# Optimization experiments

Measured on AMD Instinct MI355X. Metric: run time of the kernel, lower is better.

Reference implementation:

```python
import jax, jax.numpy as jnp
import numpy as np

L, C, S = 4096, 128, 64
SAMPLE_RATE = 4096.0  # Hz; dt offset is 1/sample_rate as in the flax module


def setup_inputs() -> dict:
    key = jax.random.key(0)
    ks = jax.random.split(key, 4)
    x = jax.random.normal(ks[0], (L, C), dtype=jnp.float32)
    # S4D-real init: A = -arange(1, S+1), param stores log(-A) broadcast to (C, S)
    A_log = jnp.broadcast_to(
        jnp.log(jnp.arange(1, S + 1, dtype=jnp.float32)), (C, S)
    )
    sc = 1.0 / np.sqrt(C)  # lecun_normal-like scale for Dense kernels
    B_kernel = (jax.random.normal(ks[1], (C, S)) * sc).astype(jnp.float32)
    B_bias = jnp.zeros((S,), jnp.float32)
    C_kernel = (jax.random.normal(ks[2], (C, S)) * sc).astype(jnp.float32)
    C_bias = jnp.zeros((S,), jnp.float32)
    dt_kernel = (jax.random.normal(ks[3], (C, C)) * sc).astype(jnp.float32)
    dt_bias = jnp.zeros((C,), jnp.float32)
    return {
        "x": x,
        "A_log": A_log,
        "B_kernel": B_kernel,
        "B_bias": B_bias,
        "C_kernel": C_kernel,
        "C_bias": C_bias,
        "dt_kernel": dt_kernel,
        "dt_bias": dt_bias,
    }


def reference(x, A_log, B_kernel, B_bias, C_kernel, C_bias, dt_kernel, dt_bias):
    # ssm params
    A = -jnp.exp(A_log)                                   # (C, S), negative real
    B = 1.0 + x @ B_kernel + B_bias                       # (L, S)
    Cm = x @ C_kernel + C_bias                            # (L, S)
    dt = jax.nn.softplus(1.0 / SAMPLE_RATE + x @ dt_kernel + dt_bias)  # (L, C)
    # discretization (ZOH for diagonal real A)
    At = jnp.exp(A[None, :, :] * dt[:, :, None])          # (L, C, S)
    ut = (At - 1.0) * (B[:, None, :] / A[None, :, :]) * x[:, :, None]  # (L, C, S)

    # parallel linear-recurrence scan: h_t = At_t * h_{t-1} + ut_t, h0 = 0
    def comb(e1, e2):
        a1, u1 = e1
        a2, u2 = e2
        return (a2 * a1, a2 * u1 + u2)

    _, ht = jax.lax.associative_scan(comb, (At, ut))      # scans over axis 0 (L)
    y = jnp.einsum("ls,lcs->lc", Cm, ht)                  # (L, C)
    return y
```

## Files before the change

kernel.cpp:

```cpp
#include <hip/hip_runtime.h>
#include <math.h>

#define LL 4096
#define CC 128
#define SS 64
#define NCH 128
#define CLEN 32
#define CS 8192
#define GW 8
#define NG 16

__global__ __launch_bounds__(256) void k_proj(
    const float* __restrict__ x,
    const float* __restrict__ Bk, const float* __restrict__ Bb,
    const float* __restrict__ Ck, const float* __restrict__ Cb,
    const float* __restrict__ Dk, const float* __restrict__ Db,
    float* __restrict__ Bmat, float* __restrict__ Cmat,
    float* __restrict__ DTmT, float* __restrict__ xT)
{
    __shared__ float xs[CC][20];
    const int r0 = blockIdx.x * 16;
    const int t = threadIdx.x;
    {
        const int r = t >> 4, k8 = (t & 15) * 8;
        const float4 v0 = *(const float4*)&x[(r0 + r) * CC + k8];
        const float4 v1 = *(const float4*)&x[(r0 + r) * CC + k8 + 4];
        xs[k8+0][r] = v0.x; xs[k8+1][r] = v0.y; xs[k8+2][r] = v0.z; xs[k8+3][r] = v0.w;
        xs[k8+4][r] = v1.x; xs[k8+5][r] = v1.y; xs[k8+6][r] = v1.z; xs[k8+7][r] = v1.w;
    }
    __syncthreads();
    {
        const int k = t >> 1, half = (t & 1) * 8;
        const float4 a = *(const float4*)&xs[k][half];
        const float4 b = *(const float4*)&xs[k][half + 4];
        *(float4*)&xT[k * LL + r0 + half]     = a;
        *(float4*)&xT[k * LL + r0 + half + 4] = b;
    }
    const int tc = t & 63, tr = t >> 6;
    const float* Wb; int wstride, wo;
    if (tc < 16)      { Wb = Bk; wstride = SS; wo = 4 * tc; }
    else if (tc < 32) { Wb = Ck; wstride = SS; wo = 4 * tc - 64; }
    else              { Wb = Dk; wstride = CC; wo = 4 * tc - 128; }
    float acc[4][4];
#pragma unroll
    for (int r = 0; r < 4; ++r)
#pragma unroll
        for (int j = 0; j < 4; ++j) acc[r][j] = 0.0f;
    for (int k = 0; k < CC; ++k) {
        const float4 wq = *(const float4*)(Wb + k * wstride + wo);
        const float4 xq = *(const float4*)&xs[k][4 * tr];
        const float wv[4] = {wq.x, wq.y, wq.z, wq.w};
        const float xv[4] = {xq.x, xq.y, xq.z, xq.w};
#pragma unroll
        for (int r = 0; r < 4; ++r)
#pragma unroll
            for (int j = 0; j < 4; ++j) acc[r][j] = fmaf(xv[r], wv[j], acc[r][j]);
    }
    const int rb = r0 + 4 * tr;
    if (tc < 32) {
        const float* bb = (tc < 16) ? Bb : Cb;
        const float add = (tc < 16) ? 1.0f : 0.0f;
        float bias[4];
#pragma unroll
        for (int j = 0; j < 4; ++j) bias[j] = add + bb[wo + j];
        float* dst = (tc < 16) ? Bmat : Cmat;
#pragma unroll
        for (int r = 0; r < 4; ++r) {
            const float4 o = make_float4(acc[r][0] + bias[0], acc[r][1] + bias[1],
                                         acc[r][2] + bias[2], acc[r][3] + bias[3]);
            *(float4*)&dst[(rb + r) * SS + wo] = o;
        }
    } else {
#pragma unroll
        for (int j = 0; j < 4; ++j) {
            const float bj = Db[wo + j] + 0.000244140625f;
            float sp[4];
#pragma unroll
            for (int r = 0; r < 4; ++r) {
                const float z = acc[r][j] + bj;
                sp[r] = fmaxf(z, 0.0f) + log1pf(__expf(-fabsf(z)));
            }
            *(float4*)&DTmT[(wo + j) * LL + rb] = make_float4(sp[0], sp[1], sp[2], sp[3]);
        }
    }
}

__global__ __launch_bounds__(512) void k_chunk(
    const float* __restrict__ xT, const float* __restrict__ A_log,
    const float* __restrict__ Bmat, const float* __restrict__ DTmT,
    float* __restrict__ Ea, float* __restrict__ Eu,
    float* __restrict__ Ga, float* __restrict__ Gu)
{
    __shared__ float2 agg[GW][SS];
    const int lane = threadIdx.x & 63;
    const int w = threadIdx.x >> 6;
    const int c = blockIdx.x >> 4;
    const int g = blockIdx.x & (NG - 1);
    const int ch = __builtin_amdgcn_readfirstlane(g * GW + w);
    const float A = -__expf(A_log[c * SS + lane]);
    const float invA = 1.0f / A;
    const int l0 = ch * CLEN;
    const float* dtp = DTmT + c * LL + l0;
    const float* xp  = xT   + c * LL + l0;
    const float* Bp  = Bmat + l0 * SS + lane;
    float ap = 1.0f, uc = 0.0f;
#pragma unroll
    for (int i = 0; i < CLEN; ++i) {
        const float dtl = dtp[i];
        const float xl  = xp[i];
        const float Bl  = Bp[i * SS];
        const float At  = __expf(A * dtl);
        const float u   = (At - 1.0f) * invA * (Bl * xl);
        ap *= At;
        uc = fmaf(At, uc, u);
    }
    agg[w][lane] = make_float2(ap, uc);
    __syncthreads();
    float ea = 1.0f, eu = 0.0f;
    for (int k = 0; k < w; ++k) {
        const float2 tt = agg[k][lane];
        eu = fmaf(tt.x, eu, tt.y);
        ea *= tt.x;
    }
    const int j = c * SS + lane;
    Ea[ch * CS + j] = ea;
    Eu[ch * CS + j] = eu;
    if (w == GW - 1) {
        const float2 tt = agg[GW - 1][lane];
        Gu[g * CS + j] = fmaf(tt.x, eu, tt.y);
        Ga[g * CS + j] = ea * tt.x;
    }
}

__global__ __launch_bounds__(256) void k_mid(
    const float* __restrict__ Ga, const float* __restrict__ Gu,
    float* __restrict__ hG)
{
    const int j = blockIdx.x * 256 + threadIdx.x;
    float h = 0.0f;
#pragma unroll
    for (int g = 0; g < NG; ++g) {
        hG[g * CS + j] = h;
        h = fmaf(Ga[g * CS + j], h, Gu[g * CS + j]);
    }
}

__global__ __launch_bounds__(256) void k_emit(
    const float* __restrict__ xT, const float* __restrict__ A_log,
    const float* __restrict__ Bmat, const float* __restrict__ Cmat,
    const float* __restrict__ DTmT,
    const float* __restrict__ Ea, const float* __restrict__ Eu,
    const float* __restrict__ hG,
    float* __restrict__ y)
{
    const int lane = threadIdx.x & 63;
    const int gw = blockIdx.x * 4 + (threadIdx.x >> 6);
    const int c  = __builtin_amdgcn_readfirstlane(gw & (CC - 1));
    const int ch = __builtin_amdgcn_readfirstlane(gw >> 7);
    const int g  = ch >> 3;
    const float A = -__expf(A_log[c * SS + lane]);
    const float invA = 1.0f / A;
    const int l0 = ch * CLEN;
    const int j = c * SS + lane;
    const float* dtp = DTmT + c * LL + l0;
    const float* xp  = xT   + c * LL + l0;
    const float* Bp  = Bmat + l0 * SS + lane;
    const float* Cp  = Cmat + l0 * SS + lane;
    float h = fmaf(Ea[ch * CS + j], hG[g * CS + j], Eu[ch * CS + j]);
    float p[CLEN];
#pragma unroll
    for (int i = 0; i < CLEN; ++i) {
        const float dtl = dtp[i];
        const float xl  = xp[i];
        const float Bl  = Bp[i * SS];
        const float Cl  = Cp[i * SS];
        const float At  = __expf(A * dtl);
        const float u   = (At - 1.0f) * invA * (Bl * xl);
        h = fmaf(At, h, u);
        p[i] = Cl * h;
    }
#pragma unroll
    for (int k = 0; k < 5; ++k) {
        const int d = 1 << k;
        const bool hi = (lane & d) != 0;
#pragma unroll
        for (int i = 0; i < (CLEN >> (k + 1)); ++i) {
            const float a = p[2 * i], b = p[2 * i + 1];
            const float send = hi ? a : b;
            const float t = __shfl_xor(send, d, 64);
            p[i] = (hi ? b : a) + t;
        }
    }
    const float t = __shfl_xor(p[0], 32, 64);
    const float yv = p[0] + t;
    if (lane < 32) y[(l0 + lane) * CC + c] = yv;
}

extern "C" void kernel_launch(void* const* d_in, const int* in_sizes, int n_in,
                              void* d_out, int out_size, void* d_ws, size_t ws_size,
                              hipStream_t stream)
{
    const float* x  = (const float*)d_in[0];
    const float* Al = (const float*)d_in[1];
    const float* Bk = (const float*)d_in[2];
    const float* Bb = (const float*)d_in[3];
    const float* Ck = (const float*)d_in[4];
    const float* Cb = (const float*)d_in[5];
    const float* Dk = (const float*)d_in[6];
    const float* Db = (const float*)d_in[7];
    float* y  = (float*)d_out;
    float* ws = (float*)d_ws;

    float* Bmat = ws;
    float* Cmat = Bmat + LL * SS;
    float* DTmT = Cmat + LL * SS;
    float* xT   = DTmT + CC * LL;
    float* Ea   = xT   + CC * LL;
    float* Eu   = Ea   + NCH * CS;
    float* Ga   = Eu   + NCH * CS;
    float* Gu   = Ga   + NG * CS;
    float* hG   = Gu   + NG * CS;

    k_proj <<<LL / 16,           256, 0, stream>>>(x, Bk, Bb, Ck, Cb, Dk, Db, Bmat, Cmat, DTmT, xT);
    k_chunk<<<CC * NG,           512, 0, stream>>>(xT, Al, Bmat, DTmT, Ea, Eu, Ga, Gu);
    k_mid  <<<CS / 256,          256, 0, stream>>>(Ga, Gu, hG);
    k_emit <<<(NCH * CS) / 256,  256, 0, stream>>>(xT, Al, Bmat, Cmat, DTmT, Ea, Eu, hG, y);
}
```

Before: 58.30 us.

## Fuse group-prefix scan into emit, drop per-chunk carries, shrink projection tiles

Removes the k_mid kernel and the Ea/Eu per-chunk buffers. k_agg now writes only group aggregates. k_emit recomputes each chunk's aggregate in shared memory, rebuilds the intra-group prefix, and serially folds the preceding group aggregates to get its starting state. This saves one launch and the global round trips of per-chunk carries, at the cost of recomputing the chunk exponentials in emit. The projection kernel now computes 4 rows per block with a 1x4 register tile instead of 16 rows with 4x4, giving more blocks but less weight reuse per load.

```diff
diff --git a/kernel.cpp b/kernel.cpp
--- a/kernel.cpp
+++ b/kernel.cpp
@@ -18,177 +18,152 @@
     float* __restrict__ Bmat, float* __restrict__ Cmat,
     float* __restrict__ DTmT, float* __restrict__ xT)
 {
-    __shared__ float xs[CC][20];
-    const int r0 = blockIdx.x * 16;
+    __shared__ float xs[CC][4];
+    const int r0 = blockIdx.x * 4;
     const int t = threadIdx.x;
     {
-        const int r = t >> 4, k8 = (t & 15) * 8;
-        const float4 v0 = *(const float4*)&x[(r0 + r) * CC + k8];
-        const float4 v1 = *(const float4*)&x[(r0 + r) * CC + k8 + 4];
-        xs[k8+0][r] = v0.x; xs[k8+1][r] = v0.y; xs[k8+2][r] = v0.z; xs[k8+3][r] = v0.w;
-        xs[k8+4][r] = v1.x; xs[k8+5][r] = v1.y; xs[k8+6][r] = v1.z; xs[k8+7][r] = v1.w;
+        const int r = t >> 6, k2 = (t & 63) * 2;
+        const float2 v = *(const float2*)&x[(r0 + r) * CC + k2];
+        xs[k2][r] = v.x; xs[k2 + 1][r] = v.y;
     }
     __syncthreads();
-    {
-        const int k = t >> 1, half = (t & 1) * 8;
-        const float4 a = *(const float4*)&xs[k][half];
-        const float4 b = *(const float4*)&xs[k][half + 4];
-        *(float4*)&xT[k * LL + r0 + half]     = a;
-        *(float4*)&xT[k * LL + r0 + half + 4] = b;
+    if (t < CC) {
+        *(float4*)&xT[t * LL + r0] = *(const float4*)&xs[t][0];
     }
     const int tc = t & 63, tr = t >> 6;
     const float* Wb; int wstride, wo;
     if (tc < 16)      { Wb = Bk; wstride = SS; wo = 4 * tc; }
     else if (tc < 32) { Wb = Ck; wstride = SS; wo = 4 * tc - 64; }
     else              { Wb = Dk; wstride = CC; wo = 4 * tc - 128; }
-    float acc[4][4];
-#pragma unroll
-    for (int r = 0; r < 4; ++r)
-#pragma unroll
-        for (int j = 0; j < 4; ++j) acc[r][j] = 0.0f;
+    float acc[4] = {0.f, 0.f, 0.f, 0.f};
+#pragma unroll 8
     for (int k = 0; k < CC; ++k) {
         const float4 wq = *(const float4*)(Wb + k * wstride + wo);
-        const float4 xq = *(const float4*)&xs[k][4 * tr];
-        const float wv[4] = {wq.x, wq.y, wq.z, wq.w};
-        const float xv[4] = {xq.x, xq.y, xq.z, xq.w};
-#pragma unroll
-        for (int r = 0; r < 4; ++r)
-#pragma unroll
-            for (int j = 0; j < 4; ++j) acc[r][j] = fmaf(xv[r], wv[j], acc[r][j]);
+        const float xv = xs[k][tr];
+        acc[0] = fmaf(xv, wq.x, acc[0]);
+        acc[1] = fmaf(xv, wq.y, acc[1]);
+        acc[2] = fmaf(xv, wq.z, acc[2]);
+        acc[3] = fmaf(xv, wq.w, acc[3]);
     }
-    const int rb = r0 + 4 * tr;
-    if (tc < 32) {
-        const float* bb = (tc < 16) ? Bb : Cb;
-        const float add = (tc < 16) ? 1.0f : 0.0f;
-        float bias[4];
-#pragma unroll
-        for (int j = 0; j < 4; ++j) bias[j] = add + bb[wo + j];
-        float* dst = (tc < 16) ? Bmat : Cmat;
-#pragma unroll
-        for (int r = 0; r < 4; ++r) {
-            const float4 o = make_float4(acc[r][0] + bias[0], acc[r][1] + bias[1],
-                                         acc[r][2] + bias[2], acc[r][3] + bias[3]);
-            *(float4*)&dst[(rb + r) * SS + wo] = o;
-        }
+    const int row = r0 + tr;
+    if (tc < 16) {
+        const float4 o = make_float4(acc[0] + 1.0f + Bb[wo], acc[1] + 1.0f + Bb[wo+1],
+                                     acc[2] + 1.0f + Bb[wo+2], acc[3] + 1.0f + Bb[wo+3]);
+        *(float4*)&Bmat[row * SS + wo] = o;
+    } else if (tc < 32) {
+        const float4 o = make_float4(acc[0] + Cb[wo], acc[1] + Cb[wo+1],
+                                     acc[2] + Cb[wo+2], acc[3] + Cb[wo+3]);
+        *(float4*)&Cmat[row * SS + wo] = o;
     } else {
 #pragma unroll
         for (int j = 0; j < 4; ++j) {
-            const float bj = Db[wo + j] + 0.000244140625f;
-            float sp[4];
-#pragma unroll
-            for (int r = 0; r < 4; ++r) {
-                const float z = acc[r][j] + bj;
-                sp[r] = fmaxf(z, 0.0f) + log1pf(__expf(-fabsf(z)));
-            }
-            *(float4*)&DTmT[(wo + j) * LL + rb] = make_float4(sp[0], sp[1], sp[2], sp[3]);
+            const float z = acc[j] + Db[wo + j] + 0.000244140625f;
+            const float sp = fmaxf(z, 0.0f) + log1pf(__expf(-fabsf(z)));
+            DTmT[(wo + j) * LL + row] = sp;
         }
     }
 }
 
-__global__ __launch_bounds__(512) void k_chunk(
+__global__ __launch_bounds__(512, 4) void k_agg(
     const float* __restrict__ xT, const float* __restrict__ A_log,
     const float* __restrict__ Bmat, const float* __restrict__ DTmT,
-    float* __restrict__ Ea, float* __restrict__ Eu,
     float* __restrict__ Ga, float* __restrict__ Gu)
 {
-    __shared__ float2 agg[GW][SS];
+    __shared__ float2 sagg[GW][SS];
     const int lane = threadIdx.x & 63;
-    const int w = threadIdx.x >> 6;
+    const int w = __builtin_amdgcn_readfirstlane(threadIdx.x >> 6);
     const int c = blockIdx.x >> 4;
     const int g = blockIdx.x & (NG - 1);
-    const int ch = __builtin_amdgcn_readfirstlane(g * GW + w);
-    const float A = -__expf(A_log[c * SS + lane]);
+    const int j = c * SS + lane;
+    const float A = -__expf(A_log[j]);
     const float invA = 1.0f / A;
-    const int l0 = ch * CLEN;
+    const int l0 = (g * GW + w) * CLEN;
     const float* dtp = DTmT + c * LL + l0;
     const float* xp  = xT   + c * LL + l0;
     const float* Bp  = Bmat + l0 * SS + lane;
     float ap = 1.0f, uc = 0.0f;
 #pragma unroll
     for (int i = 0; i < CLEN; ++i) {
-        const float dtl = dtp[i];
-        const float xl  = xp[i];
-        const float Bl  = Bp[i * SS];
-        const float At  = __expf(A * dtl);
-        const float u   = (At - 1.0f) * invA * (Bl * xl);
+        const float At = __expf(A * dtp[i]);
+        const float u  = (At - 1.0f) * invA * (Bp[i * SS] * xp[i]);
         ap *= At;
         uc = fmaf(At, uc, u);
     }
-    agg[w][lane] = make_float2(ap, uc);
+    sagg[w][lane] = make_float2(ap, uc);
     __syncthreads();
-    float ea = 1.0f, eu = 0.0f;
-    for (int k = 0; k < w; ++k) {
-        const float2 tt = agg[k][lane];
-        eu = fmaf(tt.x, eu, tt.y);
-        ea *= tt.x;
-    }
-    const int j = c * SS + lane;
-    Ea[ch * CS + j] = ea;
-    Eu[ch * CS + j] = eu;
-    if (w == GW - 1) {
-        const float2 tt = agg[GW - 1][lane];
-        Gu[g * CS + j] = fmaf(tt.x, eu, tt.y);
-        Ga[g * CS + j] = ea * tt.x;
+    if (w == 0) {
+        float ga = 1.0f, gu = 0.0f;
+#pragma unroll
+        for (int k = 0; k < GW; ++k) {
+            const float2 t = sagg[k][lane];
+            gu = fmaf(t.x, gu, t.y);
+            ga *= t.x;
+        }
+        Ga[g * CS + j] = ga;
+        Gu[g * CS + j] = gu;
     }
 }
 
-__global__ __launch_bounds__(256) void k_mid(
-    const float* __restrict__ Ga, const float* __restrict__ Gu,
-    float* __restrict__ hG)
-{
-    const int j = blockIdx.x * 256 + threadIdx.x;
-    float h = 0.0f;
-#pragma unroll
-    for (int g = 0; g < NG; ++g) {
-        hG[g * CS + j] = h;
-        h = fmaf(Ga[g * CS + j], h, Gu[g * CS + j]);
-    }
-}
-
-__global__ __launch_bounds__(256) void k_emit(
+__global__ __launch_bounds__(512, 4) void k_emit(
     const float* __restrict__ xT, const float* __restrict__ A_log,
     const float* __restrict__ Bmat, const float* __restrict__ Cmat,
     const float* __restrict__ DTmT,
-    const float* __restrict__ Ea, const float* __restrict__ Eu,
-    const float* __restrict__ hG,
+    const float* __restrict__ Ga, const float* __restrict__ Gu,
     float* __restrict__ y)
 {
+    __shared__ float2 sagg[GW][SS];
     const int lane = threadIdx.x & 63;
-    const int gw = blockIdx.x * 4 + (threadIdx.x >> 6);
-    const int c  = __builtin_amdgcn_readfirstlane(gw & (CC - 1));
-    const int ch = __builtin_amdgcn_readfirstlane(gw >> 7);
-    const int g  = ch >> 3;
-    const float A = -__expf(A_log[c * SS + lane]);
+    const int w = __builtin_amdgcn_readfirstlane(threadIdx.x >> 6);
+    const int c = blockIdx.x >> 4;
+    const int g = blockIdx.x & (NG - 1);
+    const int j = c * SS + lane;
+    const float A = -__expf(A_log[j]);
     const float invA = 1.0f / A;
-    const int l0 = ch * CLEN;
-    const int j = c * SS + lane;
+    float hg = 0.0f;
+    for (int gg = 0; gg < g; ++gg)
+        hg = fmaf(Ga[gg * CS + j], hg, Gu[gg * CS + j]);
+    const int l0 = (g * GW + w) * CLEN;
     const float* dtp = DTmT + c * LL + l0;
     const float* xp  = xT   + c * LL + l0;
     const float* Bp  = Bmat + l0 * SS + lane;
     const float* Cp  = Cmat + l0 * SS + lane;
-    float h = fmaf(Ea[ch * CS + j], hG[g * CS + j], Eu[ch * CS + j]);
+    {
+        float ap = 1.0f, uc = 0.0f;
+#pragma unroll
+        for (int i = 0; i < CLEN; ++i) {
+            const float At = __expf(A * dtp[i]);
+            const float u  = (At - 1.0f) * invA * (Bp[i * SS] * xp[i]);
+            ap *= At;
+            uc = fmaf(At, uc, u);
+        }
+        sagg[w][lane] = make_float2(ap, uc);
+    }
+    __syncthreads();
+    float ea = 1.0f, eu = 0.0f;
+    for (int k = 0; k < w; ++k) {
+        const float2 t = sagg[k][lane];
+        eu = fmaf(t.x, eu, t.y);
+        ea *= t.x;
+    }
+    float h = fmaf(ea, hg, eu);
     float p[CLEN];
 #pragma unroll
     for (int i = 0; i < CLEN; ++i) {
-        const float dtl = dtp[i];
-        const float xl  = xp[i];
-        const float Bl  = Bp[i * SS];
-        const float Cl  = Cp[i * SS];
-        const float At  = __expf(A * dtl);
-        const float u   = (At - 1.0f) * invA * (Bl * xl);
+        const float At = __expf(A * dtp[i]);
+        const float u  = (At - 1.0f) * invA * (Bp[i * SS] * xp[i]);
         h = fmaf(At, h, u);
-        p[i] = Cl * h;
+        p[i] = Cp[i * SS] * h;
     }
 #pragma unroll
     for (int k = 0; k < 5; ++k) {
         const int d = 1 << k;
         const bool hi = (lane & d) != 0;
 #pragma unroll
-        for (int i = 0; i < (CLEN >> (k + 1)); ++i) {
-            const float a = p[2 * i], b = p[2 * i + 1];
+        for (int i2 = 0; i2 < (CLEN >> (k + 1)); ++i2) {
+            const float a = p[2 * i2], b = p[2 * i2 + 1];
             const float send = hi ? a : b;
             const float t = __shfl_xor(send, d, 64);
-            p[i] = (hi ? b : a) + t;
+            p[i2] = (hi ? b : a) + t;
         }
     }
     const float t = __shfl_xor(p[0], 32, 64);
@@ -215,14 +190,10 @@
     float* Cmat = Bmat + LL * SS;
     float* DTmT = Cmat + LL * SS;
     float* xT   = DTmT + CC * LL;
-    float* Ea   = xT   + CC * LL;
-    float* Eu   = Ea   + NCH * CS;
-    float* Ga   = Eu   + NCH * CS;
+    float* Ga   = xT   + CC * LL;
     float* Gu   = Ga   + NG * CS;
-    float* hG   = Gu   + NG * CS;
 
-    k_proj <<<LL / 16,           256, 0, stream>>>(x, Bk, Bb, Ck, Cb, Dk, Db, Bmat, Cmat, DTmT, xT);
-    k_chunk<<<CC * NG,           512, 0, stream>>>(xT, Al, Bmat, DTmT, Ea, Eu, Ga, Gu);
-    k_mid  <<<CS / 256,          256, 0, stream>>>(Ga, Gu, hG);
-    k_emit <<<(NCH * CS) / 256,  256, 0, stream>>>(xT, Al, Bmat, Cmat, DTmT, Ea, Eu, hG, y);
+    k_proj<<<LL / 4,  256, 0, stream>>>(x, Bk, Bb, Ck, Cb, Dk, Db, Bmat, Cmat, DTmT, xT);
+    k_agg <<<CC * NG, 512, 0, stream>>>(xT, Al, Bmat, DTmT, Ga, Gu);
+    k_emit<<<CC * NG, 512, 0, stream>>>(xT, Al, Bmat, Cmat, DTmT, Ga, Gu, y);
 }
```

After: 65.23 us. +11.9%, slower.

## Merge mid-scan into emit kernel and drop per-chunk carry buffers

Applied to the files above, without the earlier changes.

Removes the separate group-carry kernel and the per-chunk Ea/Eu workspace arrays. The first sweep now writes only per-group aggregates. The emit kernel redoes the intra-group chunk aggregation in shared memory and serially combines up to 15 group aggregates per thread to get its starting state. This saves one launch and the global traffic for chunk carries, at the cost of recomputing chunk aggregates and extra register pressure from holding the at/uu arrays.

```diff
diff --git a/kernel.cpp b/kernel.cpp
--- a/kernel.cpp
+++ b/kernel.cpp
@@ -4,11 +4,10 @@
 #define LL 4096
 #define CC 128
 #define SS 64
-#define NCH 128
 #define CLEN 32
-#define CS 8192
 #define GW 8
 #define NG 16
+#define CS 8192
 
 __global__ __launch_bounds__(256) void k_proj(
     const float* __restrict__ x,
@@ -85,114 +84,117 @@
     }
 }
 
-__global__ __launch_bounds__(512) void k_chunk(
+__global__ __launch_bounds__(512, 4) void k_sweep1(
     const float* __restrict__ xT, const float* __restrict__ A_log,
     const float* __restrict__ Bmat, const float* __restrict__ DTmT,
-    float* __restrict__ Ea, float* __restrict__ Eu,
     float* __restrict__ Ga, float* __restrict__ Gu)
 {
     __shared__ float2 agg[GW][SS];
     const int lane = threadIdx.x & 63;
-    const int w = threadIdx.x >> 6;
+    const int w = __builtin_amdgcn_readfirstlane(threadIdx.x >> 6);
     const int c = blockIdx.x >> 4;
     const int g = blockIdx.x & (NG - 1);
-    const int ch = __builtin_amdgcn_readfirstlane(g * GW + w);
-    const float A = -__expf(A_log[c * SS + lane]);
+    const int j = c * SS + lane;
+    const float A = -__expf(A_log[j]);
     const float invA = 1.0f / A;
-    const int l0 = ch * CLEN;
+    const int l0 = (g * GW + w) * CLEN;
     const float* dtp = DTmT + c * LL + l0;
     const float* xp  = xT   + c * LL + l0;
     const float* Bp  = Bmat + l0 * SS + lane;
     float ap = 1.0f, uc = 0.0f;
 #pragma unroll
     for (int i = 0; i < CLEN; ++i) {
-        const float dtl = dtp[i];
-        const float xl  = xp[i];
-        const float Bl  = Bp[i * SS];
-        const float At  = __expf(A * dtl);
-        const float u   = (At - 1.0f) * invA * (Bl * xl);
+        const float At = __expf(A * dtp[i]);
+        const float u  = (At - 1.0f) * invA * (Bp[i * SS] * xp[i]);
         ap *= At;
         uc = fmaf(At, uc, u);
     }
     agg[w][lane] = make_float2(ap, uc);
     __syncthreads();
-    float ea = 1.0f, eu = 0.0f;
-    for (int k = 0; k < w; ++k) {
-        const float2 tt = agg[k][lane];
-        eu = fmaf(tt.x, eu, tt.y);
-        ea *= tt.x;
-    }
-    const int j = c * SS + lane;
-    Ea[ch * CS + j] = ea;
-    Eu[ch * CS + j] = eu;
-    if (w == GW - 1) {
-        const float2 tt = agg[GW - 1][lane];
-        Gu[g * CS + j] = fmaf(tt.x, eu, tt.y);
-        Ga[g * CS + j] = ea * tt.x;
-    }
-}
-
-__global__ __launch_bounds__(256) void k_mid(
-    const float* __restrict__ Ga, const float* __restrict__ Gu,
-    float* __restrict__ hG)
-{
-    const int j = blockIdx.x * 256 + threadIdx.x;
-    float h = 0.0f;
-#pragma unroll
-    for (int g = 0; g < NG; ++g) {
-        hG[g * CS + j] = h;
-        h = fmaf(Ga[g * CS + j], h, Gu[g * CS + j]);
-    }
-}
-
-__global__ __launch_bounds__(256) void k_emit(
+    if (w == 0) {
+        float ga = 1.0f, gu = 0.0f;
+#pragma unroll
+        for (int k = 0; k < GW; ++k) {
+            const float2 t = agg[k][lane];
+            gu = fmaf(t.x, gu, t.y);
+            ga *= t.x;
+        }
+        Ga[g * CS + j] = ga;
+        Gu[g * CS + j] = gu;
+    }
+}
+
+__global__ __launch_bounds__(512, 4) void k_emit(
     const float* __restrict__ xT, const float* __restrict__ A_log,
     const float* __restrict__ Bmat, const float* __restrict__ Cmat,
     const float* __restrict__ DTmT,
-    const float* __restrict__ Ea, const float* __restrict__ Eu,
-    const float* __restrict__ hG,
+    const float* __restrict__ Ga, const float* __restrict__ Gu,
     float* __restrict__ y)
 {
+    __shared__ float2 agg[GW][SS];
     const int lane = threadIdx.x & 63;
-    const int gw = blockIdx.x * 4 + (threadIdx.x >> 6);
-    const int c  = __builtin_amdgcn_readfirstlane(gw & (CC - 1));
-    const int ch = __builtin_amdgcn_readfirstlane(gw >> 7);
-    const int g  = ch >> 3;
-    const float A = -__expf(A_log[c * SS + lane]);
+    const int w = __builtin_amdgcn_readfirstlane(threadIdx.x >> 6);
+    const int c = blockIdx.x >> 4;
+    const int g = blockIdx.x & (NG - 1);
+    const int j = c * SS + lane;
+    const float A = -__expf(A_log[j]);
     const float invA = 1.0f / A;
-    const int l0 = ch * CLEN;
-    const int j = c * SS + lane;
+    float hg = 0.0f;
+    {
+        float gar[NG - 1], gur[NG - 1];
+#pragma unroll
+        for (int gg = 0; gg < NG - 1; ++gg) {
+            gar[gg] = Ga[gg * CS + j];
+            gur[gg] = Gu[gg * CS + j];
+        }
+#pragma unroll
+        for (int gg = 0; gg < NG - 1; ++gg)
+            hg = (gg < g) ? fmaf(gar[gg], hg, gur[gg]) : hg;
+    }
+    const int l0 = (g * GW + w) * CLEN;
     const float* dtp = DTmT + c * LL + l0;
     const float* xp  = xT   + c * LL + l0;
     const float* Bp  = Bmat + l0 * SS + lane;
     const float* Cp  = Cmat + l0 * SS + lane;
-    float h = fmaf(Ea[ch * CS + j], hG[g * CS + j], Eu[ch * CS + j]);
-    float p[CLEN];
+    float at[CLEN], uu[CLEN];
+    {
+        float ap = 1.0f, uc = 0.0f;
+#pragma unroll
+        for (int i = 0; i < CLEN; ++i) {
+            at[i] = __expf(A * dtp[i]);
+            uu[i] = (at[i] - 1.0f) * invA * (Bp[i * SS] * xp[i]);
+            ap *= at[i];
+            uc = fmaf(at[i], uc, uu[i]);
+        }
+        agg[w][lane] = make_float2(ap, uc);
+    }
+    __syncthreads();
+    float ea = 1.0f, eu = 0.0f;
+    for (int k = 0; k < w; ++k) {
+        const float2 t = agg[k][lane];
+        eu = fmaf(t.x, eu, t.y);
+        ea *= t.x;
+    }
+    float h = fmaf(ea, hg, eu);
 #pragma unroll
     for (int i = 0; i < CLEN; ++i) {
-        const float dtl = dtp[i];
-        const float xl  = xp[i];
-        const float Bl  = Bp[i * SS];
-        const float Cl  = Cp[i * SS];
-        const float At  = __expf(A * dtl);
-        const float u   = (At - 1.0f) * invA * (Bl * xl);
-        h = fmaf(At, h, u);
-        p[i] = Cl * h;
+        h = fmaf(at[i], h, uu[i]);
+        uu[i] = Cp[i * SS] * h;
     }
 #pragma unroll
     for (int k = 0; k < 5; ++k) {
         const int d = 1 << k;
         const bool hi = (lane & d) != 0;
 #pragma unroll
-        for (int i = 0; i < (CLEN >> (k + 1)); ++i) {
-            const float a = p[2 * i], b = p[2 * i + 1];
+        for (int i2 = 0; i2 < (CLEN >> (k + 1)); ++i2) {
+            const float a = uu[2 * i2], b = uu[2 * i2 + 1];
             const float send = hi ? a : b;
             const float t = __shfl_xor(send, d, 64);
-            p[i] = (hi ? b : a) + t;
-        }
-    }
-    const float t = __shfl_xor(p[0], 32, 64);
-    const float yv = p[0] + t;
+            uu[i2] = (hi ? b : a) + t;
+        }
+    }
+    const float t = __shfl_xor(uu[0], 32, 64);
+    const float yv = uu[0] + t;
     if (lane < 32) y[(l0 + lane) * CC + c] = yv;
 }
 
@@ -215,14 +217,10 @@
     float* Cmat = Bmat + LL * SS;
     float* DTmT = Cmat + LL * SS;
     float* xT   = DTmT + CC * LL;
-    float* Ea   = xT   + CC * LL;
-    float* Eu   = Ea   + NCH * CS;
-    float* Ga   = Eu   + NCH * CS;
+    float* Ga   = xT   + CC * LL;
     float* Gu   = Ga   + NG * CS;
-    float* hG   = Gu   + NG * CS;
-
-    k_proj <<<LL / 16,           256, 0, stream>>>(x, Bk, Bb, Ck, Cb, Dk, Db, Bmat, Cmat, DTmT, xT);
-    k_chunk<<<CC * NG,           512, 0, stream>>>(xT, Al, Bmat, DTmT, Ea, Eu, Ga, Gu);
-    k_mid  <<<CS / 256,          256, 0, stream>>>(Ga, Gu, hG);
-    k_emit <<<(NCH * CS) / 256,  256, 0, stream>>>(xT, Al, Bmat, Cmat, DTmT, Ea, Eu, hG, y);
-}
+
+    k_proj  <<<LL / 16, 256, 0, stream>>>(x, Bk, Bb, Ck, Cb, Dk, Db, Bmat, Cmat, DTmT, xT);
+    k_sweep1<<<CC * NG, 512, 0, stream>>>(xT, Al, Bmat, DTmT, Ga, Gu);
+    k_emit  <<<CC * NG, 512, 0, stream>>>(xT, Al, Bmat, Cmat, DTmT, Ga, Gu, y);
+}
```

After: 49.83 us. -14.5%, faster.
